# Kernel optimization log

Hardware: AMD Instinct MI355X
Metric: run time of the kernel (lower is better)

Reference implementation:

```python
import jax, jax.numpy as jnp
import numpy as np

N_NODES = 100000
N_EDGES = 1600000
D = 128          # h_size == feature_representation_size
N_CLASSES = 2
N_GRAPHS = 64


def setup_inputs() -> dict:
    key = jax.random.key(0)
    ks = jax.random.split(key, 8)
    scale = 1.0 / np.sqrt(D)
    x = jax.random.normal(ks[0], (N_NODES, D), jnp.float32)
    edge_index = jax.random.randint(ks[1], (2, N_EDGES), 0, N_NODES, dtype=jnp.int64)
    batch = jnp.sort(jax.random.randint(ks[2], (N_NODES,), 0, N_GRAPHS, dtype=jnp.int64))
    W0 = jax.random.normal(ks[3], (D, D), jnp.float32) * scale
    W1 = jax.random.normal(ks[4], (D, D), jnp.float32) * scale
    W2 = jax.random.normal(ks[5], (D, D), jnp.float32) * scale
    Wf = jax.random.normal(ks[6], (D, N_CLASSES), jnp.float32) * scale
    return dict(
        x=x, edge_index=edge_index, batch=batch,
        W0=W0, b0=jnp.zeros((D,), jnp.float32),
        W1=W1, b1=jnp.zeros((D,), jnp.float32),
        W2=W2, b2=jnp.zeros((D,), jnp.float32),
        Wf=Wf, bf=jnp.zeros((N_CLASSES,), jnp.float32),
    )


def gcn_norm(edge_index, num_nodes):
    # add self loops, symmetric normalization D^{-1/2} A_hat D^{-1/2}
    src, dst = edge_index[0], edge_index[1]
    loop = jnp.arange(num_nodes, dtype=src.dtype)
    src = jnp.concatenate([src, loop])
    dst = jnp.concatenate([dst, loop])
    ew = jnp.ones(src.shape[0], jnp.float32)
    deg = jax.ops.segment_sum(ew, dst, num_segments=num_nodes)
    dinv = jnp.where(deg > 0, jax.lax.rsqrt(deg), 0.0)
    norm = dinv[src] * dinv[dst]  # [E+N]
    return src, dst, norm


def gcn_conv(h, W, b, src, dst, norm, num_nodes):
    h = h @ W                                   # linear transform
    msg = h[src] * norm[:, None]                # gather + scale over edges
    out = jax.ops.segment_sum(msg, dst, num_segments=num_nodes)  # scatter-add
    return out + b


def reference(x, edge_index, batch, W0, b0, W1, b1, W2, b2, Wf, bf):
    n = x.shape[0]
    src, dst, norm = gcn_norm(edge_index, n)
    h = jax.nn.relu(gcn_conv(x, W0, b0, src, dst, norm, n))
    h = jax.nn.relu(gcn_conv(h, W1, b1, src, dst, norm, n))
    h = gcn_conv(h, W2, b2, src, dst, norm, n)  # last layer, no relu
    pooled = jax.ops.segment_max(h, batch, num_segments=N_GRAPHS)  # global max pool
    return pooled @ Wf + bf
```

## Files before the change

kernel.cpp:

```cpp
#include <hip/hip_runtime.h>
#include <hip/hip_bf16.h>
#include <hip/hip_fp16.h>
#include <float.h>

#define D 128
#define NGRAPHS 64
#define BKSHIFT 9
#define BKNODES 512
#define MAXBK 256
#define PCH 2048
#define HCH 4096

typedef _Float16 h8 __attribute__((ext_vector_type(8)));
typedef float f4 __attribute__((ext_vector_type(4)));

__device__ __forceinline__ unsigned fkey(float f){
  unsigned u = __float_as_uint(f);
  return (u & 0x80000000u) ? ~u : (u | 0x80000000u);
}
__device__ __forceinline__ float funkey(unsigned k){
  unsigned u = (k & 0x80000000u) ? (k ^ 0x80000000u) : ~k;
  return __uint_as_float(u);
}

__device__ __forceinline__ void wcvt_pair(const float* __restrict__ W,
    _Float16* __restrict__ dstp, int pair, int lane){
  int quad = lane >> 4;
  int n    = lane & 15;
  int k0 = pair >> 3;
  int tt = pair & 7;
  _Float16 v[8];
  #pragma unroll
  for (int j = 0; j < 8; j++){
    int k = k0 * 32 + quad * 8 + j;
    v[j] = (_Float16)W[k * 128 + 16 * tt + n];
  }
  *(uint4*)&dstp[((size_t)pair * 64 + lane) * 8] = *(uint4*)v;
}

__global__ __launch_bounds__(256) void k_wcvt0h(const float* __restrict__ W0,
    _Float16* __restrict__ Wsw, const int* __restrict__ dst,
    int* __restrict__ bcnt, int E){
  __shared__ int h[MAXBK];
  if (blockIdx.x < 8){
    int lane = threadIdx.x & 63;
    int pair = blockIdx.x * 4 + (threadIdx.x >> 6);
    wcvt_pair(W0, Wsw, pair, lane);
    return;
  }
  int t = threadIdx.x;
  for (int i = t; i < MAXBK; i += 256) h[i] = 0;
  __syncthreads();
  int e0 = (blockIdx.x - 8) * HCH;
  #pragma unroll
  for (int j = 0; j < HCH / 256; j++){
    int e = e0 + t + j * 256;
    if (e < E) atomicAdd(&h[dst[e] >> BKSHIFT], 1);
  }
  __syncthreads();
  for (int i = t; i < MAXBK; i += 256) if (h[i]) atomicAdd(&bcnt[i], h[i]);
}

__global__ __launch_bounds__(256) void k_mega2(
    const float* __restrict__ x, const _Float16* __restrict__ Wsw0,
    _Float16* __restrict__ C, int M, int gb,
    const int* __restrict__ src, const int* __restrict__ dst,
    const int* __restrict__ bcnt, int* __restrict__ bCur,
    uint2* __restrict__ epart, int E, int npart,
    const float* __restrict__ W1, const float* __restrict__ W2,
    _Float16* __restrict__ Wsw12){
  __shared__ __align__(16) char smraw[5120 + PCH * 8];
  int bid = blockIdx.x;
  if (bid < gb){
    _Float16 (*lds)[136] = (_Float16(*)[136])(smraw + (threadIdx.x >> 6) * 16 * 136 * 2);
    int lane = threadIdx.x & 63;
    int quad = lane >> 4;
    int l15  = lane & 15;
    int m0 = bid * 64 + (threadIdx.x >> 6) * 16;
    if (m0 >= M) return;
    f4 acc[8] = {};
    h8 af[4];
    const float* arow = x + (size_t)(m0 + l15) * D;
    #pragma unroll
    for (int k0 = 0; k0 < 4; k0++){
      float4 a = *(const float4*)&arow[k0 * 32 + quad * 8];
      float4 b = *(const float4*)&arow[k0 * 32 + quad * 8 + 4];
      __half2 p0 = __floats2half2_rn(a.x, a.y);
      __half2 p1 = __floats2half2_rn(a.z, a.w);
      __half2 p2 = __floats2half2_rn(b.x, b.y);
      __half2 p3 = __floats2half2_rn(b.z, b.w);
      union { uint4 u; h8 v; } cv;
      cv.u.x = *(unsigned*)&p0; cv.u.y = *(unsigned*)&p1;
      cv.u.z = *(unsigned*)&p2; cv.u.w = *(unsigned*)&p3;
      af[k0] = cv.v;
    }
    #pragma unroll
    for (int k0 = 0; k0 < 4; k0++){
      #pragma unroll
      for (int t = 0; t < 8; t++){
        h8 bf = *(const h8*)&Wsw0[((size_t)(k0 * 8 + t) * 64 + lane) * 8];
        acc[t] = __builtin_amdgcn_mfma_f32_16x16x32_f16(af[k0], bf, acc[t], 0, 0, 0);
      }
    }
    #pragma unroll
    for (int t = 0; t < 8; t++){
      #pragma unroll
      for (int r = 0; r < 4; r++)
        lds[quad * 4 + r][t * 16 + l15] = (_Float16)acc[t][r];
    }
    #pragma unroll
    for (int it = 0; it < 4; it++){
      int idx = it * 64 + lane;
      int row = idx >> 4;
      int ch  = idx & 15;
      *(uint4*)&C[(size_t)(m0 + row) * D + ch * 8] = *(uint4*)&lds[row][ch * 8];
    }
    return;
  }
  bid -= gb;
  if (bid < npart){
    int* scnt  = (int*)smraw;
    int* soff  = (int*)(smraw + 1024);
    int* sbase = (int*)(smraw + 2048);
    int* scur  = (int*)(smraw + 3072);
    int* stmp  = (int*)(smraw + 4096);
    uint2* stage = (uint2*)(smraw + 5120);
    int t = threadIdx.x;
    int bv = bcnt[t];
    stmp[t] = bv; __syncthreads();
    for (int off = 1; off < 256; off <<= 1){
      int xv = (t >= off) ? stmp[t - off] : 0;
      __syncthreads();
      stmp[t] += xv;
      __syncthreads();
    }
    int boffl = stmp[t] - bv;
    __syncthreads();
    int e0 = bid * PCH;
    int eN = E - e0; if (eN > PCH) eN = PCH;
    for (int i = t; i < MAXBK; i += 256){ scnt[i] = 0; scur[i] = 0; }
    __syncthreads();
    uint2 mye[PCH / 256];
    #pragma unroll
    for (int j = 0; j < PCH / 256; j++){
      int e = e0 + t + j * 256;
      if (e < E){
        mye[j].x = (unsigned)src[e];
        mye[j].y = (unsigned)dst[e];
        atomicAdd(&scnt[mye[j].y >> BKSHIFT], 1);
      }
    }
    __syncthreads();
    int v = scnt[t];
    stmp[t] = v; __syncthreads();
    for (int off = 1; off < 256; off <<= 1){
      int xv = (t >= off) ? stmp[t - off] : 0;
      __syncthreads();
      stmp[t] += xv;
      __syncthreads();
    }
    soff[t] = stmp[t] - v;
    if (v > 0) sbase[t] = boffl + atomicAdd(&bCur[t], v);
    __syncthreads();
    #pragma unroll
    for (int j = 0; j < PCH / 256; j++){
      int e = e0 + t + j * 256;
      if (e < E){
        int b = mye[j].y >> BKSHIFT;
        int l = atomicAdd(&scur[b], 1);
        stage[soff[b] + l] = mye[j];
      }
    }
    __syncthreads();
    for (int j = t; j < eN; j += 256){
      uint2 ed = stage[j];
      int b = (int)(ed.y >> BKSHIFT);
      epart[(size_t)sbase[b] + (j - soff[b])] = ed;
    }
    return;
  }
  bid -= npart;
  const float* W = (bid < 2) ? W1 : W2;
  _Float16* dstp = Wsw12 + ((bid < 2) ? 0 : 16384);
  int pbase = (bid & 1) * 16;
  int lane = threadIdx.x & 63;
  for (int pp = (threadIdx.x >> 6); pp < 16; pp += 4)
    wcvt_pair(W, dstp, pbase + pp, lane);
}

__global__ __launch_bounds__(512) void k_bfill(const uint2* __restrict__ epart,
    const int* __restrict__ bcnt, int* __restrict__ row_ptr,
    int* __restrict__ col, float* __restrict__ dinv, int N, int E){
  __shared__ int hc[BKNODES], cur[BKNODES];
  __shared__ int stmp[512];
  int b = blockIdx.x, t = threadIdx.x;
  int bv = (t < MAXBK) ? bcnt[t] : 0;
  stmp[t] = bv; __syncthreads();
  for (int o = 1; o < 512; o <<= 1){
    int xv = (t >= o) ? stmp[t - o] : 0;
    __syncthreads();
    stmp[t] += xv;
    __syncthreads();
  }
  int cntE = bcnt[b];
  int base = stmp[b] - cntE;
  __syncthreads();
  if (b == (int)gridDim.x - 1 && t == 0) row_ptr[N] = E;
  int node0 = b << BKSHIFT;
  int nloc = N - node0; if (nloc > BKNODES) nloc = BKNODES;
  hc[t] = 0;
  __syncthreads();
  for (int j = t; j < cntE; j += 512){
    uint2 ed = epart[(size_t)base + j];
    atomicAdd(&hc[ed.y - node0], 1);
  }
  __syncthreads();
  int s = hc[t];
  stmp[t] = s; __syncthreads();
  for (int o = 1; o < 512; o <<= 1){
    int xv = (t >= o) ? stmp[t - o] : 0;
    __syncthreads();
    stmp[t] += xv;
    __syncthreads();
  }
  int ex = stmp[t] - s;
  if (t < nloc){
    row_ptr[node0 + t] = base + ex;
    dinv[node0 + t]    = rsqrtf((float)s + 1.0f);
  }
  cur[t] = ex;
  __syncthreads();
  for (int j = t; j < cntE; j += 512){
    uint2 ed = epart[(size_t)base + j];
    int p = atomicAdd(&cur[ed.y - node0], 1);
    col[base + p] = (int)ed.x;
  }
}

__device__ __forceinline__ void accm(float* acc, uint4 u, float w){
  union { uint4 u; _Float16 h[8]; } cv;
  cv.u = u;
  #pragma unroll
  for (int k = 0; k < 8; k++)
    acc[k] += (float)cv.h[k] * w;
}

__global__ __launch_bounds__(256) void k_agg(const __half* __restrict__ t,
    const int* __restrict__ row_ptr, const int* __restrict__ col,
    const float* __restrict__ dinv, const float* __restrict__ bias,
    __half* __restrict__ outh, int relu, int N){
  int node = blockIdx.x * 4 + (threadIdx.x >> 6);
  if (node >= N) return;
  int lane = threadIdx.x & 63;
  int way  = lane >> 4;
  int cg   = (lane & 15) * 8;
  float di = dinv[node];
  int beg = row_ptr[node], end = row_ptr[node + 1];
  float acc[8] = {0.f,0.f,0.f,0.f,0.f,0.f,0.f,0.f};
  int j = beg + way;
  for (; j + 12 < end; j += 16){
    int s0 = col[j], s1 = col[j + 4], s2 = col[j + 8], s3 = col[j + 12];
    float w0 = dinv[s0] * di;
    float w1 = dinv[s1] * di;
    float w2 = dinv[s2] * di;
    float w3 = dinv[s3] * di;
    uint4 u0 = *(const uint4*)&t[(size_t)s0 * D + cg];
    uint4 u1 = *(const uint4*)&t[(size_t)s1 * D + cg];
    uint4 u2 = *(const uint4*)&t[(size_t)s2 * D + cg];
    uint4 u3 = *(const uint4*)&t[(size_t)s3 * D + cg];
    accm(acc, u0, w0);
    accm(acc, u1, w1);
    accm(acc, u2, w2);
    accm(acc, u3, w3);
  }
  for (; j < end; j += 4){
    int s = col[j];
    float w = dinv[s] * di;
    uint4 u = *(const uint4*)&t[(size_t)s * D + cg];
    accm(acc, u, w);
  }
  #pragma unroll
  for (int k = 0; k < 8; k++){
    acc[k] += __shfl_xor(acc[k], 16, 64);
    acc[k] += __shfl_xor(acc[k], 32, 64);
  }
  if (way == 0){
    uint4 su = *(const uint4*)&t[(size_t)node * D + cg];
    union { uint4 u; _Float16 h[8]; } sv; sv.u = su;
    float dii = di * di;
    float4 b0 = *(const float4*)&bias[cg];
    float4 b1 = *(const float4*)&bias[cg + 4];
    float bb[8] = {b0.x, b0.y, b0.z, b0.w, b1.x, b1.y, b1.z, b1.w};
    float o[8];
    #pragma unroll
    for (int k = 0; k < 8; k++)
      o[k] = acc[k] + (float)sv.h[k] * dii + bb[k];
    if (relu){
      #pragma unroll
      for (int k = 0; k < 8; k++) o[k] = fmaxf(o[k], 0.f);
    }
    __half2 p0 = __floats2half2_rn(o[0], o[1]);
    __half2 p1 = __floats2half2_rn(o[2], o[3]);
    __half2 p2 = __floats2half2_rn(o[4], o[5]);
    __half2 p3 = __floats2half2_rn(o[6], o[7]);
    uint4 u;
    u.x = *(unsigned*)&p0; u.y = *(unsigned*)&p1;
    u.z = *(unsigned*)&p2; u.w = *(unsigned*)&p3;
    *(uint4*)&outh[(size_t)node * D + cg] = u;
  }
}

__global__ __launch_bounds__(256) void k_aggs(const __half* __restrict__ t,
    const int* __restrict__ row_ptr, const int* __restrict__ col,
    const float* __restrict__ dinv, const float* __restrict__ bias,
    __half* __restrict__ outh, int relu, int N){
  int node = blockIdx.x * 4 + (threadIdx.x >> 6);
  if (node >= N) return;
  int lane = threadIdx.x & 63;
  int way  = lane >> 4;
  int cg   = (lane & 15) * 8;
  float di = dinv[node];
  int beg = row_ptr[node], end = row_ptr[node + 1];
  float acc[8] = {0.f,0.f,0.f,0.f,0.f,0.f,0.f,0.f};
  int j = beg + way;
  for (; j + 12 < end; j += 16){
    int s0 = col[j], s1 = col[j + 4], s2 = col[j + 8], s3 = col[j + 12];
    uint4 u0 = *(const uint4*)&t[(size_t)s0 * D + cg];
    uint4 u1 = *(const uint4*)&t[(size_t)s1 * D + cg];
    uint4 u2 = *(const uint4*)&t[(size_t)s2 * D + cg];
    uint4 u3 = *(const uint4*)&t[(size_t)s3 * D + cg];
    accm(acc, u0, di);
    accm(acc, u1, di);
    accm(acc, u2, di);
    accm(acc, u3, di);
  }
  for (; j < end; j += 4){
    int s = col[j];
    uint4 u = *(const uint4*)&t[(size_t)s * D + cg];
    accm(acc, u, di);
  }
  #pragma unroll
  for (int k = 0; k < 8; k++){
    acc[k] += __shfl_xor(acc[k], 16, 64);
    acc[k] += __shfl_xor(acc[k], 32, 64);
  }
  if (way == 0){
    uint4 su = *(const uint4*)&t[(size_t)node * D + cg];
    union { uint4 u; _Float16 h[8]; } sv; sv.u = su;
    float4 b0 = *(const float4*)&bias[cg];
    float4 b1 = *(const float4*)&bias[cg + 4];
    float bb[8] = {b0.x, b0.y, b0.z, b0.w, b1.x, b1.y, b1.z, b1.w};
    float o[8];
    #pragma unroll
    for (int k = 0; k < 8; k++)
      o[k] = acc[k] + (float)sv.h[k] * di + bb[k];
    if (relu){
      #pragma unroll
      for (int k = 0; k < 8; k++) o[k] = fmaxf(o[k], 0.f);
    }
    __half2 p0 = __floats2half2_rn(o[0], o[1]);
    __half2 p1 = __floats2half2_rn(o[2], o[3]);
    __half2 p2 = __floats2half2_rn(o[4], o[5]);
    __half2 p3 = __floats2half2_rn(o[6], o[7]);
    uint4 u;
    u.x = *(unsigned*)&p0; u.y = *(unsigned*)&p1;
    u.z = *(unsigned*)&p2; u.w = *(unsigned*)&p3;
    *(uint4*)&outh[(size_t)node * D + cg] = u;
  }
}

__global__ __launch_bounds__(256) void gemm_mfma(const _Float16* __restrict__ A,
    const _Float16* __restrict__ Wsw, const float* __restrict__ dinv,
    _Float16* __restrict__ C, int M){
  __shared__ _Float16 lds[4][16][136];
  int wave = threadIdx.x >> 6;
  int lane = threadIdx.x & 63;
  int quad = lane >> 4;
  int l15  = lane & 15;
  int m0 = blockIdx.x * 64 + wave * 16;
  if (m0 >= M) return;
  f4 acc[8] = {};
  h8 af[4];
  const _Float16* arow = A + (size_t)(m0 + l15) * D;
  #pragma unroll
  for (int k0 = 0; k0 < 4; k0++)
    af[k0] = *(const h8*)&arow[k0 * 32 + quad * 8];
  #pragma unroll
  for (int k0 = 0; k0 < 4; k0++){
    #pragma unroll
    for (int t = 0; t < 8; t++){
      h8 bf = *(const h8*)&Wsw[((size_t)(k0 * 8 + t) * 64 + lane) * 8];
      acc[t] = __builtin_amdgcn_mfma_f32_16x16x32_f16(af[k0], bf, acc[t], 0, 0, 0);
    }
  }
  float dv[4];
  #pragma unroll
  for (int r = 0; r < 4; r++){
    int gr = m0 + quad * 4 + r;
    dv[r] = (gr < M) ? dinv[gr] : 0.f;
  }
  #pragma unroll
  for (int t = 0; t < 8; t++){
    #pragma unroll
    for (int r = 0; r < 4; r++)
      lds[wave][quad * 4 + r][t * 16 + l15] = (_Float16)(acc[t][r] * dv[r]);
  }
  #pragma unroll
  for (int it = 0; it < 4; it++){
    int idx = it * 64 + lane;
    int row = idx >> 4;
    int ch  = idx & 15;
    *(uint4*)&C[(size_t)(m0 + row) * D + ch * 8] = *(uint4*)&lds[wave][row][ch * 8];
  }
}

__global__ __launch_bounds__(128) void k_pool(const __half* __restrict__ h,
    const int* __restrict__ batch, unsigned* __restrict__ pk, int N){
  int d = threadIdx.x;
  int n0 = blockIdx.x * 64;
  int nEnd = n0 + 64; if (nEnd > N) nEnd = N;
  float cur = -FLT_MAX;
  int curg = batch[n0];
  int n = n0;
  for (; n + 3 < nEnd; n += 4){
    const __half* r = &h[(size_t)n * D + d];
    __half v0 = r[0], v1 = r[D], v2 = r[2 * D], v3 = r[3 * D];
    int g0 = batch[n], g1 = batch[n + 1], g2 = batch[n + 2], g3 = batch[n + 3];
    if (g0 != curg){ atomicMax(&pk[curg * D + d], fkey(cur)); cur = -FLT_MAX; curg = g0; }
    cur = fmaxf(cur, __half2float(v0));
    if (g1 != curg){ atomicMax(&pk[curg * D + d], fkey(cur)); cur = -FLT_MAX; curg = g1; }
    cur = fmaxf(cur, __half2float(v1));
    if (g2 != curg){ atomicMax(&pk[curg * D + d], fkey(cur)); cur = -FLT_MAX; curg = g2; }
    cur = fmaxf(cur, __half2float(v2));
    if (g3 != curg){ atomicMax(&pk[curg * D + d], fkey(cur)); cur = -FLT_MAX; curg = g3; }
    cur = fmaxf(cur, __half2float(v3));
  }
  for (; n < nEnd; n++){
    int g = batch[n];
    if (g != curg){ atomicMax(&pk[curg * D + d], fkey(cur)); cur = -FLT_MAX; curg = g; }
    cur = fmaxf(cur, __half2float(h[(size_t)n * D + d]));
  }
  atomicMax(&pk[curg * D + d], fkey(cur));
}

__global__ __launch_bounds__(128) void k_final(const unsigned* __restrict__ pk,
    const float* __restrict__ Wf, const float* __restrict__ bf,
    float* __restrict__ out){
  int t = threadIdx.x;
  int g = t >> 1, c = t & 1;
  float s = bf[c];
  for (int k = 0; k < D; k++)
    s += funkey(pk[g * D + k]) * Wf[k * 2 + c];
  out[g * 2 + c] = s;
}

extern "C" void kernel_launch(void* const* d_in, const int* in_sizes, int n_in,
                              void* d_out, int out_size, void* d_ws, size_t ws_size,
                              hipStream_t stream){
  const float* x   = (const float*)d_in[0];
  const int*   ei  = (const int*)d_in[1];
  const int*   bat = (const int*)d_in[2];
  const float* W0  = (const float*)d_in[3];
  const float* b0  = (const float*)d_in[4];
  const float* W1  = (const float*)d_in[5];
  const float* b1  = (const float*)d_in[6];
  const float* W2  = (const float*)d_in[7];
  const float* b2  = (const float*)d_in[8];
  const float* Wf  = (const float*)d_in[9];
  const float* bf  = (const float*)d_in[10];
  int N = in_sizes[0] / D;
  int E = in_sizes[1] / 2;
  const int* srcp = ei;
  const int* dstp = ei + E;
  int nbk   = (N + BKNODES - 1) / BKNODES;
  int npart = (E + PCH - 1) / PCH;
  int nh    = (E + HCH - 1) / HCH;
  int gb    = (N + 63) / 64;

  char* p = (char*)d_ws;
  auto alloc = [&](size_t bytes)->char*{
    char* r = p; p += (bytes + 255) & ~(size_t)255; return r;
  };
  float*     dinv    = (float*)alloc((size_t)N * 4);
  int*       row_ptr = (int*)alloc((size_t)(N + 1) * 4);
  int*       col     = (int*)alloc((size_t)E * 4);
  uint2*     epart   = (uint2*)alloc((size_t)E * 8);
  _Float16*  tmp     = (_Float16*)alloc((size_t)N * D * 2);
  _Float16*  tmp2    = (_Float16*)alloc((size_t)N * D * 2);
  _Float16*  Wsw     = (_Float16*)alloc((size_t)3 * 16384 * 2);
  unsigned*  pk      = (unsigned*)alloc((size_t)NGRAPHS * D * 4);
  int*       bcnt    = (int*)alloc((size_t)MAXBK * 4);
  int*       bCur    = (int*)alloc((size_t)MAXBK * 4);

  hipMemsetAsync(pk, 0, 32768 + 1024 + 1024, stream);
  k_wcvt0h<<<8 + nh, 256, 0, stream>>>(W0, Wsw, dstp, bcnt, E);
  k_mega2<<<gb + npart + 4, 256, 0, stream>>>(x, Wsw, tmp, N, gb,
      srcp, dstp, bcnt, bCur, epart, E, npart, W1, W2, Wsw + 16384);
  k_bfill<<<nbk, 512, 0, stream>>>(epart, bcnt, row_ptr, col, dinv, N, E);

  int ablocks = (N + 3) / 4;
  k_agg<<<ablocks, 256, 0, stream>>>((const __half*)tmp, row_ptr, col, dinv, b0, (__half*)tmp2, 1, N);
  gemm_mfma<<<gb, 256, 0, stream>>>(tmp2, Wsw + 16384, dinv, tmp, N);
  k_aggs<<<ablocks, 256, 0, stream>>>((const __half*)tmp, row_ptr, col, dinv, b1, (__half*)tmp2, 1, N);
  gemm_mfma<<<gb, 256, 0, stream>>>(tmp2, Wsw + 32768, dinv, tmp, N);
  k_aggs<<<ablocks, 256, 0, stream>>>((const __half*)tmp, row_ptr, col, dinv, b2, (__half*)tmp2, 0, N);
  k_pool<<<(N + 63) / 64, 128, 0, stream>>>((const __half*)tmp2, bat, pk, N);
  k_final<<<1, 128, 0, stream>>>(pk, Wf, bf, (float*)d_out);
}
```

Baseline: 404.0 us.

## Compute degrees early, prescale first GEMM by dinv, fuse pooling into last aggregation

Per-node in-degree is now counted with global atomics in the histogram kernel and dinv is computed up front. This lets the first GEMM output be prescaled by dinv so layer 1 can use the cheaper pre-scaled aggregation kernel. The edge partition is packed into 32-bit words (20-bit source plus local dst), which halves its traffic, and bfill no longer needs its own counting pass. The final aggregation applies max-pooling directly with atomicMax, removing the k_pool kernel and the tmp2 write. The cost is 1.6M global atomics on cnt, an extra small kernel launch, and heavy atomicMax contention on the 64x128 pool buffer.

```diff
diff --git a/kernel.cpp b/kernel.cpp
--- a/kernel.cpp
+++ b/kernel.cpp
@@ -40,7 +40,7 @@
 
 __global__ __launch_bounds__(256) void k_wcvt0h(const float* __restrict__ W0,
     _Float16* __restrict__ Wsw, const int* __restrict__ dst,
-    int* __restrict__ bcnt, int E){
+    int* __restrict__ bcnt, int* __restrict__ cnt, int E){
   __shared__ int h[MAXBK];
   if (blockIdx.x < 8){
     int lane = threadIdx.x & 63;
@@ -55,18 +55,28 @@
   #pragma unroll
   for (int j = 0; j < HCH / 256; j++){
     int e = e0 + t + j * 256;
-    if (e < E) atomicAdd(&h[dst[e] >> BKSHIFT], 1);
+    if (e < E){
+      int d = dst[e];
+      atomicAdd(&h[d >> BKSHIFT], 1);
+      atomicAdd(&cnt[d], 1);
+    }
   }
   __syncthreads();
   for (int i = t; i < MAXBK; i += 256) if (h[i]) atomicAdd(&bcnt[i], h[i]);
 }
 
+__global__ __launch_bounds__(256) void k_dinv(const int* __restrict__ cnt,
+    float* __restrict__ dinv, int N){
+  int i = blockIdx.x * 256 + threadIdx.x;
+  if (i < N) dinv[i] = rsqrtf((float)cnt[i] + 1.0f);
+}
+
 __global__ __launch_bounds__(256) void k_mega2(
     const float* __restrict__ x, const _Float16* __restrict__ Wsw0,
-    _Float16* __restrict__ C, int M, int gb,
+    const float* __restrict__ dinv, _Float16* __restrict__ C, int M, int gb,
     const int* __restrict__ src, const int* __restrict__ dst,
     const int* __restrict__ bcnt, int* __restrict__ bCur,
-    uint2* __restrict__ epart, int E, int npart,
+    unsigned* __restrict__ epart, int E, int npart,
     const float* __restrict__ W1, const float* __restrict__ W2,
     _Float16* __restrict__ Wsw12){
   __shared__ __align__(16) char smraw[5120 + PCH * 8];
@@ -102,11 +112,17 @@
         acc[t] = __builtin_amdgcn_mfma_f32_16x16x32_f16(af[k0], bf, acc[t], 0, 0, 0);
       }
     }
+    float dv[4];
+    #pragma unroll
+    for (int r = 0; r < 4; r++){
+      int gr = m0 + quad * 4 + r;
+      dv[r] = (gr < M) ? dinv[gr] : 0.f;
+    }
     #pragma unroll
     for (int t = 0; t < 8; t++){
       #pragma unroll
       for (int r = 0; r < 4; r++)
-        lds[quad * 4 + r][t * 16 + l15] = (_Float16)acc[t][r];
+        lds[quad * 4 + r][t * 16 + l15] = (_Float16)(acc[t][r] * dv[r]);
     }
     #pragma unroll
     for (int it = 0; it < 4; it++){
@@ -175,7 +191,8 @@
     for (int j = t; j < eN; j += 256){
       uint2 ed = stage[j];
       int b = (int)(ed.y >> BKSHIFT);
-      epart[(size_t)sbase[b] + (j - soff[b])] = ed;
+      unsigned pw = ed.x | ((ed.y & (BKNODES - 1)) << 20);
+      epart[(size_t)sbase[b] + (j - soff[b])] = pw;
     }
     return;
   }
@@ -188,10 +205,10 @@
     wcvt_pair(W, dstp, pbase + pp, lane);
 }
 
-__global__ __launch_bounds__(512) void k_bfill(const uint2* __restrict__ epart,
-    const int* __restrict__ bcnt, int* __restrict__ row_ptr,
-    int* __restrict__ col, float* __restrict__ dinv, int N, int E){
-  __shared__ int hc[BKNODES], cur[BKNODES];
+__global__ __launch_bounds__(512) void k_bfill(const unsigned* __restrict__ epart,
+    const int* __restrict__ bcnt, const int* __restrict__ cnt,
+    int* __restrict__ row_ptr, int* __restrict__ col, int N, int E){
+  __shared__ int cur[BKNODES];
   __shared__ int stmp[512];
   int b = blockIdx.x, t = threadIdx.x;
   int bv = (t < MAXBK) ? bcnt[t] : 0;
@@ -208,32 +225,23 @@
   if (b == (int)gridDim.x - 1 && t == 0) row_ptr[N] = E;
   int node0 = b << BKSHIFT;
   int nloc = N - node0; if (nloc > BKNODES) nloc = BKNODES;
-  hc[t] = 0;
+  int c = (t < nloc) ? cnt[node0 + t] : 0;
+  stmp[t] = c; __syncthreads();
+  for (int o = 1; o < 512; o <<= 1){
+    int xv = (t >= o) ? stmp[t - o] : 0;
+    __syncthreads();
+    stmp[t] += xv;
+    __syncthreads();
+  }
+  int ex = stmp[t] - c;
+  if (t < nloc) row_ptr[node0 + t] = base + ex;
+  cur[t] = base + ex;
   __syncthreads();
   for (int j = t; j < cntE; j += 512){
-    uint2 ed = epart[(size_t)base + j];
-    atomicAdd(&hc[ed.y - node0], 1);
-  }
-  __syncthreads();
-  int s = hc[t];
-  stmp[t] = s; __syncthreads();
-  for (int o = 1; o < 512; o <<= 1){
-    int xv = (t >= o) ? stmp[t - o] : 0;
-    __syncthreads();
-    stmp[t] += xv;
-    __syncthreads();
-  }
-  int ex = stmp[t] - s;
-  if (t < nloc){
-    row_ptr[node0 + t] = base + ex;
-    dinv[node0 + t]    = rsqrtf((float)s + 1.0f);
-  }
-  cur[t] = ex;
-  __syncthreads();
-  for (int j = t; j < cntE; j += 512){
-    uint2 ed = epart[(size_t)base + j];
-    int p = atomicAdd(&cur[ed.y - node0], 1);
-    col[base + p] = (int)ed.x;
+    unsigned pw = epart[(size_t)base + j];
+    int dloc = (int)(pw >> 20);
+    int p = atomicAdd(&cur[dloc], 1);
+    col[p] = (int)(pw & 0xFFFFFu);
   }
 }
 
@@ -243,71 +251,6 @@
   #pragma unroll
   for (int k = 0; k < 8; k++)
     acc[k] += (float)cv.h[k] * w;
-}
-
-__global__ __launch_bounds__(256) void k_agg(const __half* __restrict__ t,
-    const int* __restrict__ row_ptr, const int* __restrict__ col,
-    const float* __restrict__ dinv, const float* __restrict__ bias,
-    __half* __restrict__ outh, int relu, int N){
-  int node = blockIdx.x * 4 + (threadIdx.x >> 6);
-  if (node >= N) return;
-  int lane = threadIdx.x & 63;
-  int way  = lane >> 4;
-  int cg   = (lane & 15) * 8;
-  float di = dinv[node];
-  int beg = row_ptr[node], end = row_ptr[node + 1];
-  float acc[8] = {0.f,0.f,0.f,0.f,0.f,0.f,0.f,0.f};
-  int j = beg + way;
-  for (; j + 12 < end; j += 16){
-    int s0 = col[j], s1 = col[j + 4], s2 = col[j + 8], s3 = col[j + 12];
-    float w0 = dinv[s0] * di;
-    float w1 = dinv[s1] * di;
-    float w2 = dinv[s2] * di;
-    float w3 = dinv[s3] * di;
-    uint4 u0 = *(const uint4*)&t[(size_t)s0 * D + cg];
-    uint4 u1 = *(const uint4*)&t[(size_t)s1 * D + cg];
-    uint4 u2 = *(const uint4*)&t[(size_t)s2 * D + cg];
-    uint4 u3 = *(const uint4*)&t[(size_t)s3 * D + cg];
-    accm(acc, u0, w0);
-    accm(acc, u1, w1);
-    accm(acc, u2, w2);
-    accm(acc, u3, w3);
-  }
-  for (; j < end; j += 4){
-    int s = col[j];
-    float w = dinv[s] * di;
-    uint4 u = *(const uint4*)&t[(size_t)s * D + cg];
-    accm(acc, u, w);
-  }
-  #pragma unroll
-  for (int k = 0; k < 8; k++){
-    acc[k] += __shfl_xor(acc[k], 16, 64);
-    acc[k] += __shfl_xor(acc[k], 32, 64);
-  }
-  if (way == 0){
-    uint4 su = *(const uint4*)&t[(size_t)node * D + cg];
-    union { uint4 u; _Float16 h[8]; } sv; sv.u = su;
-    float dii = di * di;
-    float4 b0 = *(const float4*)&bias[cg];
-    float4 b1 = *(const float4*)&bias[cg + 4];
-    float bb[8] = {b0.x, b0.y, b0.z, b0.w, b1.x, b1.y, b1.z, b1.w};
-    float o[8];
-    #pragma unroll
-    for (int k = 0; k < 8; k++)
-      o[k] = acc[k] + (float)sv.h[k] * dii + bb[k];
-    if (relu){
-      #pragma unroll
-      for (int k = 0; k < 8; k++) o[k] = fmaxf(o[k], 0.f);
-    }
-    __half2 p0 = __floats2half2_rn(o[0], o[1]);
-    __half2 p1 = __floats2half2_rn(o[2], o[3]);
-    __half2 p2 = __floats2half2_rn(o[4], o[5]);
-    __half2 p3 = __floats2half2_rn(o[6], o[7]);
-    uint4 u;
-    u.x = *(unsigned*)&p0; u.y = *(unsigned*)&p1;
-    u.z = *(unsigned*)&p2; u.w = *(unsigned*)&p3;
-    *(uint4*)&outh[(size_t)node * D + cg] = u;
-  }
 }
 
 __global__ __launch_bounds__(256) void k_aggs(const __half* __restrict__ t,
@@ -369,6 +312,56 @@
   }
 }
 
+__global__ __launch_bounds__(256) void k_aggsm(const __half* __restrict__ t,
+    const int* __restrict__ row_ptr, const int* __restrict__ col,
+    const float* __restrict__ dinv, const float* __restrict__ bias,
+    const int* __restrict__ batch, unsigned* __restrict__ pk, int N){
+  int node = blockIdx.x * 4 + (threadIdx.x >> 6);
+  if (node >= N) return;
+  int lane = threadIdx.x & 63;
+  int way  = lane >> 4;
+  int cg   = (lane & 15) * 8;
+  float di = dinv[node];
+  int beg = row_ptr[node], end = row_ptr[node + 1];
+  float acc[8] = {0.f,0.f,0.f,0.f,0.f,0.f,0.f,0.f};
+  int j = beg + way;
+  for (; j + 12 < end; j += 16){
+    int s0 = col[j], s1 = col[j + 4], s2 = col[j + 8], s3 = col[j + 12];
+    uint4 u0 = *(const uint4*)&t[(size_t)s0 * D + cg];
+    uint4 u1 = *(const uint4*)&t[(size_t)s1 * D + cg];
+    uint4 u2 = *(const uint4*)&t[(size_t)s2 * D + cg];
+    uint4 u3 = *(const uint4*)&t[(size_t)s3 * D + cg];
+    accm(acc, u0, di);
+    accm(acc, u1, di);
+    accm(acc, u2, di);
+    accm(acc, u3, di);
+  }
+  for (; j < end; j += 4){
+    int s = col[j];
+    uint4 u = *(const uint4*)&t[(size_t)s * D + cg];
+    accm(acc, u, di);
+  }
+  #pragma unroll
+  for (int k = 0; k < 8; k++){
+    acc[k] += __shfl_xor(acc[k], 16, 64);
+    acc[k] += __shfl_xor(acc[k], 32, 64);
+  }
+  if (way == 0){
+    uint4 su = *(const uint4*)&t[(size_t)node * D + cg];
+    union { uint4 u; _Float16 h[8]; } sv; sv.u = su;
+    float4 b0 = *(const float4*)&bias[cg];
+    float4 b1 = *(const float4*)&bias[cg + 4];
+    float bb[8] = {b0.x, b0.y, b0.z, b0.w, b1.x, b1.y, b1.z, b1.w};
+    int g = batch[node];
+    unsigned* pp = &pk[(unsigned)g * D + cg];
+    #pragma unroll
+    for (int k = 0; k < 8; k++){
+      float o = acc[k] + (float)sv.h[k] * di + bb[k];
+      atomicMax(&pp[k], fkey(o));
+    }
+  }
+}
+
 __global__ __launch_bounds__(256) void gemm_mfma(const _Float16* __restrict__ A,
     const _Float16* __restrict__ Wsw, const float* __restrict__ dinv,
     _Float16* __restrict__ C, int M){
@@ -412,35 +405,6 @@
     int ch  = idx & 15;
     *(uint4*)&C[(size_t)(m0 + row) * D + ch * 8] = *(uint4*)&lds[wave][row][ch * 8];
   }
-}
-
-__global__ __launch_bounds__(128) void k_pool(const __half* __restrict__ h,
-    const int* __restrict__ batch, unsigned* __restrict__ pk, int N){
-  int d = threadIdx.x;
-  int n0 = blockIdx.x * 64;
-  int nEnd = n0 + 64; if (nEnd > N) nEnd = N;
-  float cur = -FLT_MAX;
-  int curg = batch[n0];
-  int n = n0;
-  for (; n + 3 < nEnd; n += 4){
-    const __half* r = &h[(size_t)n * D + d];
-    __half v0 = r[0], v1 = r[D], v2 = r[2 * D], v3 = r[3 * D];
-    int g0 = batch[n], g1 = batch[n + 1], g2 = batch[n + 2], g3 = batch[n + 3];
-    if (g0 != curg){ atomicMax(&pk[curg * D + d], fkey(cur)); cur = -FLT_MAX; curg = g0; }
-    cur = fmaxf(cur, __half2float(v0));
-    if (g1 != curg){ atomicMax(&pk[curg * D + d], fkey(cur)); cur = -FLT_MAX; curg = g1; }
-    cur = fmaxf(cur, __half2float(v1));
-    if (g2 != curg){ atomicMax(&pk[curg * D + d], fkey(cur)); cur = -FLT_MAX; curg = g2; }
-    cur = fmaxf(cur, __half2float(v2));
-    if (g3 != curg){ atomicMax(&pk[curg * D + d], fkey(cur)); cur = -FLT_MAX; curg = g3; }
-    cur = fmaxf(cur, __half2float(v3));
-  }
-  for (; n < nEnd; n++){
-    int g = batch[n];
-    if (g != curg){ atomicMax(&pk[curg * D + d], fkey(cur)); cur = -FLT_MAX; curg = g; }
-    cur = fmaxf(cur, __half2float(h[(size_t)n * D + d]));
-  }
-  atomicMax(&pk[curg * D + d], fkey(cur));
 }
 
 __global__ __launch_bounds__(128) void k_final(const unsigned* __restrict__ pk,
@@ -484,26 +448,28 @@
   float*     dinv    = (float*)alloc((size_t)N * 4);
   int*       row_ptr = (int*)alloc((size_t)(N + 1) * 4);
   int*       col     = (int*)alloc((size_t)E * 4);
-  uint2*     epart   = (uint2*)alloc((size_t)E * 8);
+  unsigned*  epart   = (unsigned*)alloc((size_t)E * 4);
   _Float16*  tmp     = (_Float16*)alloc((size_t)N * D * 2);
   _Float16*  tmp2    = (_Float16*)alloc((size_t)N * D * 2);
   _Float16*  Wsw     = (_Float16*)alloc((size_t)3 * 16384 * 2);
   unsigned*  pk      = (unsigned*)alloc((size_t)NGRAPHS * D * 4);
   int*       bcnt    = (int*)alloc((size_t)MAXBK * 4);
   int*       bCur    = (int*)alloc((size_t)MAXBK * 4);
-
-  hipMemsetAsync(pk, 0, 32768 + 1024 + 1024, stream);
-  k_wcvt0h<<<8 + nh, 256, 0, stream>>>(W0, Wsw, dstp, bcnt, E);
-  k_mega2<<<gb + npart + 4, 256, 0, stream>>>(x, Wsw, tmp, N, gb,
+  int*       cnt     = (int*)alloc((size_t)N * 4);
+
+  size_t zeroB = 32768 + 1024 + 1024 + (((size_t)N * 4 + 255) & ~(size_t)255);
+  hipMemsetAsync(pk, 0, zeroB, stream);
+  k_wcvt0h<<<8 + nh, 256, 0, stream>>>(W0, Wsw, dstp, bcnt, cnt, E);
+  k_dinv<<<(N + 255) / 256, 256, 0, stream>>>(cnt, dinv, N);
+  k_mega2<<<gb + npart + 4, 256, 0, stream>>>(x, Wsw, dinv, tmp, N, gb,
       srcp, dstp, bcnt, bCur, epart, E, npart, W1, W2, Wsw + 16384);
-  k_bfill<<<nbk, 512, 0, stream>>>(epart, bcnt, row_ptr, col, dinv, N, E);
+  k_bfill<<<nbk, 512, 0, stream>>>(epart, bcnt, cnt, row_ptr, col, N, E);
 
   int ablocks = (N + 3) / 4;
-  k_agg<<<ablocks, 256, 0, stream>>>((const __half*)tmp, row_ptr, col, dinv, b0, (__half*)tmp2, 1, N);
+  k_aggs<<<ablocks, 256, 0, stream>>>((const __half*)tmp, row_ptr, col, dinv, b0, (__half*)tmp2, 1, N);
   gemm_mfma<<<gb, 256, 0, stream>>>(tmp2, Wsw + 16384, dinv, tmp, N);
   k_aggs<<<ablocks, 256, 0, stream>>>((const __half*)tmp, row_ptr, col, dinv, b1, (__half*)tmp2, 1, N);
   gemm_mfma<<<gb, 256, 0, stream>>>(tmp2, Wsw + 32768, dinv, tmp, N);
-  k_aggs<<<ablocks, 256, 0, stream>>>((const __half*)tmp, row_ptr, col, dinv, b2, (__half*)tmp2, 0, N);
-  k_pool<<<(N + 63) / 64, 128, 0, stream>>>((const __half*)tmp2, bat, pk, N);
+  k_aggsm<<<ablocks, 256, 0, stream>>>((const __half*)tmp, row_ptr, col, dinv, b2, bat, pk, N);
   k_final<<<1, 128, 0, stream>>>(pk, Wf, bf, (float*)d_out);
 }
```

Measured after the change: 1.389 ms. 244% more time.
